# Performance work log

Hardware: AMD Instinct MI355X
Metric: run time of the kernel (lower is better)

## Reference

```python
import jax, jax.numpy as jnp
import numpy as np

B, S, D = 4, 2048, 768
H = 12
DH = D // H  # 64
DF = 2048
THETA = 10000.0
EPS = 1e-5


def setup_inputs() -> dict:
    key = jax.random.key(0)
    ks = jax.random.split(key, 8)
    sc = 0.02  # keep activations numerically tame
    return {
        "x": jax.random.normal(ks[0], (B, S, D), jnp.float32),
        "ln1_w": jnp.ones((D,), jnp.float32),
        "ln2_w": jnp.ones((D,), jnp.float32),
        "p_q": jax.random.normal(ks[1], (D, D), jnp.float32) * sc,
        "p_k": jax.random.normal(ks[2], (D, D), jnp.float32) * sc,
        "p_v": jax.random.normal(ks[3], (D, D), jnp.float32) * sc,
        "p_o": jax.random.normal(ks[4], (D, D), jnp.float32) * sc,
        "w1": jax.random.normal(ks[5], (DF, D), jnp.float32) * sc,
        "w2": jax.random.normal(ks[6], (D, DF), jnp.float32) * sc,
        "w3": jax.random.normal(ks[7], (DF, D), jnp.float32) * sc,
    }


def _rmsnorm(x, w):
    # matches torch: fp32 compute, mean-square + eps
    rms = jnp.sqrt(jnp.mean(x * x, axis=-1, keepdims=True) + EPS)
    return x / rms * w


def _rope(t):
    # t: [B, H, S, DH]; rotation per RoPE matrix: pairs (2k, 2k+1)
    pos = jnp.arange(S, dtype=jnp.float32)[:, None]            # [S,1]
    k = jnp.arange(DH // 2, dtype=jnp.float32)[None, :]        # [1,DH/2]
    ang = pos / (THETA ** (2.0 * k / DH))                      # [S,DH/2]
    cos, sin = jnp.cos(ang), jnp.sin(ang)
    t2 = t.reshape(*t.shape[:-1], DH // 2, 2)
    x0, x1 = t2[..., 0], t2[..., 1]
    o0 = cos * x0 - sin * x1
    o1 = sin * x0 + cos * x1
    return jnp.stack([o0, o1], axis=-1).reshape(t.shape)


def reference(x, ln1_w, ln2_w, p_q, p_k, p_v, p_o, w1, w2, w3):
    # --- attention sublayer ---
    h = _rmsnorm(x, ln1_w)                                     # [B,S,D]
    Wq = p_q.reshape(H, DH, D)
    Wk = p_k.reshape(H, DH, D)
    Wv = p_v.reshape(H, DH, D)
    q = _rope(jnp.einsum('bsd,hed->bhse', h, Wq))              # [B,H,S,DH]
    k = _rope(jnp.einsum('bsd,hed->bhse', h, Wk))
    v = jnp.einsum('bsd,hed->bhse', h, Wv)
    scores = jnp.einsum('bhqe,bhke->bhqk', q, k)               # [B,H,S,S]
    mask = jnp.tril(jnp.ones((S, S), bool))
    scores = jnp.where(mask, scores, -jnp.inf)
    attn = jax.nn.softmax(scores / jnp.sqrt(jnp.float32(DH)), axis=-1)
    ctx = jnp.einsum('bhqk,bhke->bhqe', attn, v)               # [B,H,S,DH]
    ctx = jnp.transpose(ctx, (0, 2, 1, 3)).reshape(B, S, D)    # [B,S,D]
    x = x + ctx @ p_o.T
    # --- SwiGLU FFN sublayer ---
    h2 = _rmsnorm(x, ln2_w)
    u1 = h2 @ w1.T
    u1 = u1 * jax.nn.sigmoid(u1)                               # SiLU
    u3 = h2 @ w3.T
    x = x + (u1 * u3) @ w2.T
    return x
```

## Files before the change

### kernel.cpp

```cpp
#include <hip/hip_runtime.h>
#include <stdint.h>

#define B_  4
#define S_  2048
#define D_  768
#define H_  12
#define DH_ 64
#define DF_ 2048
#define M_  (B_*S_)
#define NQKV 2304
#define N13  4096

typedef __attribute__((ext_vector_type(8))) short bf16x8;
typedef __attribute__((ext_vector_type(4))) short bf16x4;
typedef __attribute__((ext_vector_type(4))) float f32x4;
typedef unsigned short u16;

#if !defined(__HIP_DEVICE_COMPILE__)
  #define MFMA_K16(A,B,C) (C)
#elif __has_builtin(__builtin_amdgcn_mfma_f32_16x16x16_bf16)
  #define MFMA_K16(A,B,C) __builtin_amdgcn_mfma_f32_16x16x16_bf16((A),(B),(C),0,0,0)
#else
  #define MFMA_K16(A,B,C) __builtin_amdgcn_mfma_f32_16x16x16bf16_1k((A),(B),(C),0,0,0)
#endif

__device__ __forceinline__ float bf2f(u16 v) {
  union { uint32_t u; float f; } x; x.u = ((uint32_t)v) << 16; return x.f;
}
__device__ __forceinline__ u16 f2bf(float f) {
  union { float f; uint32_t u; } x; x.f = f;
  uint32_t r = x.u + 0x7FFFu + ((x.u >> 16) & 1u);
  return (u16)(r >> 16);
}
__device__ __forceinline__ void gl_lds16(const u16* g, u16* l) {
  __builtin_amdgcn_global_load_lds((const __attribute__((address_space(1))) uint32_t*)g,
                                   (__attribute__((address_space(3))) uint32_t*)l, 16, 0, 0);
}

__global__ __launch_bounds__(256) void cast_all_kernel(const float* __restrict__ pq,
                                                       const float* __restrict__ pk,
                                                       const float* __restrict__ pv,
                                                       const float* __restrict__ po,
                                                       const float* __restrict__ w2,
                                                       u16* __restrict__ wqkv,
                                                       u16* __restrict__ wob,
                                                       u16* __restrict__ w2b) {
  int bidx = blockIdx.x;
  const float* src; u16* dst; int off;
  if (bidx < 576)       { src = pq; dst = wqkv;           off = bidx; }
  else if (bidx < 1152) { src = pk; dst = wqkv + 589824;  off = bidx - 576; }
  else if (bidx < 1728) { src = pv; dst = wqkv + 1179648; off = bidx - 1152; }
  else if (bidx < 2304) { src = po; dst = wob;            off = bidx - 1728; }
  else                  { src = w2; dst = w2b;            off = bidx - 2304; }
  int i = off * 256 + threadIdx.x;
  float4 v = ((const float4*)src)[i];
  ushort4 o;
  o.x = f2bf(v.x); o.y = f2bf(v.y); o.z = f2bf(v.z); o.w = f2bf(v.w);
  ((ushort4*)dst)[i] = o;
}

__global__ __launch_bounds__(192) void cast_w13_kernel(const float* __restrict__ w1,
                                                       const float* __restrict__ w3,
                                                       u16* __restrict__ out) {
  int j = blockIdx.x, which = blockIdx.y;
  const float* src = (which ? w3 : w1) + (size_t)j * D_;
  int fr = (j >> 4) * 32 + (j & 15) + which * 16;
  u16* dst = out + (size_t)fr * D_;
  int t = threadIdx.x;
  float4 v = ((const float4*)src)[t];
  ushort4 o;
  o.x = f2bf(v.x); o.y = f2bf(v.y); o.z = f2bf(v.z); o.w = f2bf(v.w);
  ((ushort4*)dst)[t] = o;
}

__global__ __launch_bounds__(256) void rmsnorm_kernel(const float* __restrict__ x,
                                                      const float* __restrict__ w,
                                                      u16* __restrict__ out) {
  int row = blockIdx.x, tid = threadIdx.x;
  const float* xr = x + (size_t)row * D_;
  float v0 = xr[tid], v1 = xr[tid + 256], v2 = xr[tid + 512];
  float ss = v0 * v0 + v1 * v1 + v2 * v2;
  #pragma unroll
  for (int m = 32; m >= 1; m >>= 1) ss += __shfl_xor(ss, m, 64);
  __shared__ float red[4];
  if ((tid & 63) == 0) red[tid >> 6] = ss;
  __syncthreads();
  float tot = red[0] + red[1] + red[2] + red[3];
  float r = rsqrtf(tot * (1.0f / D_) + 1e-5f);
  u16* o = out + (size_t)row * D_;
  o[tid]       = f2bf(v0 * r * w[tid]);
  o[tid + 256] = f2bf(v1 * r * w[tid + 256]);
  o[tid + 512] = f2bf(v2 * r * w[tid + 512]);
}

template<int MT, int EPI>
__global__ __launch_bounds__(256) void gemm_bt_kernel(const u16* __restrict__ A,
                                                      const u16* __restrict__ W,
                                                      void* __restrict__ Cout,
                                                      const float* __restrict__ res,
                                                      u16* __restrict__ vTout,
                                                      int K, int N) {
  constexpr int ABELEMS = MT * 64 + 128 * 64;
  constexpr int SMELEMS = (EPI == 3 && 128 * 132 > ABELEMS) ? 128 * 132 : ABELEMS;
  __shared__ __align__(16) u16 smem[SMELEMS];
  u16* As = smem;
  u16* Bs = smem + MT * 64;
  constexpr int MI = MT / 32;
  int tid = threadIdx.x;
  int wave = tid >> 6, lane = tid & 63;
  int quad = lane >> 4, l16 = lane & 15;
  int wr = (wave >> 1) * (MT / 2), wc = (wave & 1) * 64;
  int m0 = blockIdx.y * MT, n0 = blockIdx.x * 128;
  f32x4 acc[MI][4] = {};
  for (int kt = 0; kt < K; kt += 64) {
    __syncthreads();
    #pragma unroll
    for (int i = 0; i < MT / 32; ++i) {
      int idx = i * 256 + tid;
      int r = idx >> 3, c = idx & 7;
      gl_lds16(&A[(size_t)(m0 + r) * K + kt + ((c ^ (r & 7)) * 8)], &As[(i * 256 + wave * 64) * 8]);
    }
    #pragma unroll
    for (int i = 0; i < 4; ++i) {
      int idx = i * 256 + tid;
      int r = idx >> 3, c = idx & 7;
      gl_lds16(&W[(size_t)(n0 + r) * K + kt + ((c ^ (r & 7)) * 8)], &Bs[(i * 256 + wave * 64) * 8]);
    }
    __syncthreads();
    #pragma unroll
    for (int ks = 0; ks < 2; ++ks) {
      bf16x8 af[MI], bf[4];
      int sw = ((ks * 4 + quad) ^ (l16 & 7)) * 8;
      #pragma unroll
      for (int t = 0; t < MI; ++t)
        af[t] = *(const bf16x8*)&As[(wr + t * 16 + l16) * 64 + sw];
      #pragma unroll
      for (int t = 0; t < 4; ++t)
        bf[t] = *(const bf16x8*)&Bs[(wc + t * 16 + l16) * 64 + sw];
      #pragma unroll
      for (int mt = 0; mt < MI; ++mt)
        #pragma unroll
        for (int nt = 0; nt < 4; ++nt)
          acc[mt][nt] = __builtin_amdgcn_mfma_f32_16x16x32_bf16(af[mt], bf[nt], acc[mt][nt], 0, 0, 0);
    }
  }

  if (EPI == 3 && n0 >= 1536) {
    __syncthreads();
    #pragma unroll
    for (int mt = 0; mt < MI; ++mt) {
      int sloc = wr + mt * 16 + quad * 4;
      #pragma unroll
      for (int nt = 0; nt < 4; ++nt) {
        int col = wc + nt * 16 + l16;
        ushort4 o;
        o.x = f2bf(acc[mt][nt][0]); o.y = f2bf(acc[mt][nt][1]);
        o.z = f2bf(acc[mt][nt][2]); o.w = f2bf(acc[mt][nt][3]);
        *(ushort4*)&smem[col * 132 + sloc] = o;
      }
    }
    __syncthreads();
    int b = m0 >> 11, sblk = m0 & 2047;
    #pragma unroll
    for (int i = 0; i < 8; ++i) {
      int idx = i * 256 + tid;
      int row = idx >> 4, c16 = idx & 15;
      uint4 d = *(const uint4*)&smem[row * 132 + c16 * 8];
      int vg = n0 - 1536 + row;
      int h = vg >> 6, dh = vg & 63;
      *(uint4*)&vTout[((size_t)(b * H_ + h) * 64 + dh) * (size_t)S_ + sblk + c16 * 8] = d;
    }
  } else if (EPI == 3) {
    bool isq = (n0 < 768);
    float osc = isq ? 0.18033688f : 1.0f;
    #pragma unroll
    for (int mt = 0; mt < MI; ++mt) {
      int r0 = m0 + wr + mt * 16 + quad * 4;
      int pos0 = r0 & 2047;
      #pragma unroll
      for (int nt = 0; nt < 4; ++nt) {
        int col = n0 + wc + nt * 16 + l16;
        int kk = (col & 63) >> 1;
        float freq = exp2f(-0.41524101186092035f * (float)kk);
        bool odd = (col & 1);
        #pragma unroll
        for (int r = 0; r < 4; ++r) {
          float own = acc[mt][nt][r];
          float pv = __shfl_xor(own, 1, 64);
          float ang = (float)(pos0 + r) * freq;
          float sv, cv;
          __sincosf(ang, &sv, &cv);
          float o = odd ? (sv * pv + cv * own) : (cv * own - sv * pv);
          ((u16*)Cout)[(size_t)(r0 + r) * N + col] = f2bf(o * osc);
        }
      }
    }
  } else {
    #pragma unroll
    for (int mt = 0; mt < MI; ++mt) {
      #pragma unroll
      for (int r = 0; r < 4; ++r) {
        int gr = m0 + wr + mt * 16 + quad * 4 + r;
        if (EPI == 2) {
          #pragma unroll
          for (int np = 0; np < 2; ++np) {
            float u1v = acc[mt][np * 2][r], u3v = acc[mt][np * 2 + 1][r];
            float sg = 1.0f / (1.0f + __builtin_amdgcn_exp2f(-u1v * 1.44269504f));
            float g = u1v * sg * u3v;
            int gc = (n0 >> 1) + (wave & 1) * 32 + np * 16 + l16;
            ((u16*)Cout)[(size_t)gr * (N >> 1) + gc] = f2bf(g);
          }
        } else {
          #pragma unroll
          for (int nt = 0; nt < 4; ++nt) {
            int gc = n0 + wc + nt * 16 + l16;
            size_t off = (size_t)gr * N + gc;
            float vv = acc[mt][nt][r];
            if (EPI == 1) ((float*)Cout)[off] = vv + res[off];
            else          ((u16*)Cout)[off] = f2bf(vv);
          }
        }
      }
    }
  }
}

#define FENCE() asm volatile("" ::: "memory")
#define BAR() do { FENCE(); __builtin_amdgcn_s_barrier(); FENCE(); } while (0)
#define LGKM0() do { asm volatile("s_waitcnt lgkmcnt(0)" ::: "memory"); \
                     __builtin_amdgcn_sched_barrier(0); } while (0)

template<int MH, int NH>
__device__ __forceinline__ void quad_mfma(f32x4 (&acc)[2][4][2][2],
                                          const bf16x8 (&ra)[4][2],
                                          const bf16x8 (&rb)[2][2]) {
  #pragma unroll
  for (int ks = 0; ks < 2; ++ks)
    #pragma unroll
    for (int mt = 0; mt < 4; ++mt)
      #pragma unroll
      for (int nt = 0; nt < 2; ++nt)
        acc[MH][mt][NH][nt] =
          __builtin_amdgcn_mfma_f32_16x16x32_bf16(ra[mt][ks], rb[nt][ks], acc[MH][mt][NH][nt], 0, 0, 0);
}

__device__ __forceinline__ void ld_af(bf16x8 (&rr)[4][2], const u16* base,
                                      int wrow, int l16, int quad) {
  #pragma unroll
  for (int mt = 0; mt < 4; ++mt)
    #pragma unroll
    for (int ks = 0; ks < 2; ++ks)
      rr[mt][ks] = *(const bf16x8*)&base[(wrow + mt * 16 + l16) * 64 +
                                         (((ks * 4 + quad) ^ (l16 & 7)) * 8)];
}
__device__ __forceinline__ void ld_bf(bf16x8 (&rr)[2][2], const u16* base,
                                      int wrow, int l16, int quad) {
  #pragma unroll
  for (int nt = 0; nt < 2; ++nt)
    #pragma unroll
    for (int ks = 0; ks < 2; ++ks)
      rr[nt][ks] = *(const bf16x8*)&base[(wrow + nt * 16 + l16) * 64 +
                                         (((ks * 4 + quad) ^ (l16 & 7)) * 8)];
}

template<int EPI, int K, int N>
__global__ __launch_bounds__(512, 2) void gemm256_kernel(const u16* __restrict__ A,
                                                         const u16* __restrict__ W,
                                                         void* __restrict__ Cout,
                                                         const float* __restrict__ res) {
  __shared__ __align__(16) u16 smem[2][2][2][128 * 64];
  int tid = threadIdx.x;
  int wave = tid >> 6, lane = tid & 63;
  int quad = lane >> 4, l16 = lane & 15;
  int wm = wave >> 2, wn = wave & 3;
  int m0 = blockIdx.y * 256, n0 = blockIdx.x * 256;
  constexpr int NI = (K >> 6) >> 1;

  f32x4 acc[2][4][2][2] = {};
  bf16x8 rA[4][2], rBlo[2][2], rBhi[2][2];

  int r0 = tid >> 3, c0 = tid & 7;
  int scb = (c0 ^ (r0 & 7)) * 16;
  uint32_t offA = (uint32_t)(m0 + r0) * (uint32_t)(K * 2) + (uint32_t)scb;
  uint32_t offB = (uint32_t)(n0 + r0) * (uint32_t)(K * 2) + (uint32_t)scb;

  #define STG(kof, ab, h, bufi) do {                                               \
    const char* _s = (ab) ? (const char*)W : (const char*)A;                       \
    uint32_t _o = ((ab) ? offB : offA) + (uint32_t)((kof) + (h) * (128 * K * 2));  \
    u16* _d = &smem[bufi][ab][h][wave * 512];                                      \
    gl_lds16((const u16*)(_s + _o), _d);                                           \
    gl_lds16((const u16*)(_s + _o + 64 * K * 2), _d + 4096);                       \
  } while (0)

  int wrA = wm * 64, wrB = wn * 32;

  STG(0, 0, 0, 0); STG(0, 1, 0, 0); STG(0, 1, 1, 0); STG(0, 0, 1, 0);
  STG(128, 0, 0, 1); STG(128, 1, 0, 1); STG(128, 1, 1, 1); STG(128, 0, 1, 1);
  offA += 256; offB += 256;
  asm volatile("s_waitcnt vmcnt(8)" ::: "memory");
  BAR();
  ld_af(rA,   &smem[0][0][0][0], wrA, l16, quad);
  ld_bf(rBlo, &smem[0][1][0][0], wrB, l16, quad);
  LGKM0();
  BAR();

  #define G256_ITER(MORE) do {                                                     \
                                                                     \
    ld_bf(rBhi, &smem[0][1][1][0], wrB, l16, quad);                                \
    if (MORE) STG(0, 0, 0, 0);                                                     \
    BAR(); LGKM0();                                                                \
    __builtin_amdgcn_s_setprio(1); quad_mfma<0, 0>(acc, rA, rBlo);                 \
    __builtin_amdgcn_s_setprio(0); BAR();                                          \
                                                   \
    if (MORE) STG(0, 1, 0, 0);                                                     \
    BAR(); LGKM0();                                                                \
    __builtin_amdgcn_s_setprio(1); quad_mfma<0, 1>(acc, rA, rBhi);                 \
    __builtin_amdgcn_s_setprio(0);                                                 \
    ld_af(rA, &smem[0][0][1][0], wrA, l16, quad);                                  \
    BAR();                                                                         \
                                                   \
    if (MORE) STG(0, 1, 1, 0);                                                     \
    BAR(); LGKM0();                                                                \
    __builtin_amdgcn_s_setprio(1); quad_mfma<1, 0>(acc, rA, rBlo);                 \
    __builtin_amdgcn_s_setprio(0);                                                 \
    if (MORE) asm volatile("s_waitcnt vmcnt(6)" ::: "memory");                     \
    else      asm volatile("s_waitcnt vmcnt(0)" ::: "memory");                     \
    BAR();                                                                         \
                                    \
    ld_bf(rBlo, &smem[1][1][0][0], wrB, l16, quad);                                \
    if (MORE) STG(0, 0, 1, 0);                                                     \
    BAR(); LGKM0();                                                                \
    __builtin_amdgcn_s_setprio(1); quad_mfma<1, 1>(acc, rA, rBhi);                 \
    __builtin_amdgcn_s_setprio(0);                                                 \
    ld_af(rA, &smem[1][0][0][0], wrA, l16, quad);                                  \
    BAR();                                                                         \
                                                                \
    ld_bf(rBhi, &smem[1][1][1][0], wrB, l16, quad);                                \
    if (MORE) STG(128, 0, 0, 1);                                                   \
    BAR(); LGKM0();                                                                \
    __builtin_amdgcn_s_setprio(1); quad_mfma<0, 0>(acc, rA, rBlo);                 \
    __builtin_amdgcn_s_setprio(0); BAR();                                          \
                                                   \
    if (MORE) STG(128, 1, 0, 1);                                                   \
    BAR(); LGKM0();                                                                \
    __builtin_amdgcn_s_setprio(1); quad_mfma<0, 1>(acc, rA, rBhi);                 \
    __builtin_amdgcn_s_setprio(0);                                                 \
    ld_af(rA, &smem[1][0][1][0], wrA, l16, quad);                                  \
    BAR();                                                                         \
                                                   \
    if (MORE) STG(128, 1, 1, 1);                                                   \
    BAR(); LGKM0();                                                                \
    __builtin_amdgcn_s_setprio(1); quad_mfma<1, 0>(acc, rA, rBlo);                 \
    __builtin_amdgcn_s_setprio(0);                                                 \
    if (MORE) asm volatile("s_waitcnt vmcnt(6)" ::: "memory");                     \
    else      asm volatile("s_waitcnt vmcnt(0)" ::: "memory");                     \
    BAR();                                                                         \
                                    \
    if (MORE) ld_bf(rBlo, &smem[0][1][0][0], wrB, l16, quad);                      \
    if (MORE) STG(128, 0, 1, 1);                                                   \
    BAR(); LGKM0();                                                                \
    __builtin_amdgcn_s_setprio(1); quad_mfma<1, 1>(acc, rA, rBhi);                 \
    __builtin_amdgcn_s_setprio(0);                                                 \
    if (MORE) ld_af(rA, &smem[0][0][0][0], wrA, l16, quad);                        \
    BAR();                                                                         \
  } while (0)

  #pragma unroll 1
  for (int i = 0; i < NI - 1; ++i) {
    G256_ITER(true);
    offA += 256; offB += 256;
  }
  G256_ITER(false);
  #undef G256_ITER
  #undef STG

  if (EPI == 2) {
    const int Nh = N >> 1;
    #pragma unroll
    for (int mh = 0; mh < 2; ++mh)
      #pragma unroll
      for (int mt = 0; mt < 4; ++mt)
        #pragma unroll
        for (int r = 0; r < 4; ++r) {
          int gr = m0 + mh * 128 + wm * 64 + mt * 16 + quad * 4 + r;
          #pragma unroll
          for (int nh = 0; nh < 2; ++nh) {
            float u1v = acc[mh][mt][nh][0][r], u3v = acc[mh][mt][nh][1][r];
            float sg = 1.0f / (1.0f + __builtin_amdgcn_exp2f(-u1v * 1.44269504f));
            float g = u1v * sg * u3v;
            int gc = (n0 >> 1) + nh * 64 + wn * 16 + l16;
            ((u16*)Cout)[(size_t)gr * Nh + gc] = f2bf(g);
          }
        }
  } else if (EPI == 1) {
    #pragma unroll
    for (int mh = 0; mh < 2; ++mh)
      #pragma unroll
      for (int mt = 0; mt < 4; ++mt)
        #pragma unroll
        for (int r = 0; r < 4; ++r) {
          int gr = m0 + mh * 128 + wm * 64 + mt * 16 + quad * 4 + r;
          #pragma unroll
          for (int nh = 0; nh < 2; ++nh)
            #pragma unroll
            for (int nt = 0; nt < 2; ++nt) {
              int gc = n0 + nh * 128 + wn * 32 + nt * 16 + l16;
              size_t off = (size_t)gr * N + gc;
              ((float*)Cout)[off] = acc[mh][mt][nh][nt][r] + res[off];
            }
        }
  } else {
    #pragma unroll
    for (int mh = 0; mh < 2; ++mh)
      #pragma unroll
      for (int mt = 0; mt < 4; ++mt)
        #pragma unroll
        for (int r = 0; r < 4; ++r) {
          int gr = m0 + mh * 128 + wm * 64 + mt * 16 + quad * 4 + r;
          #pragma unroll
          for (int nh = 0; nh < 2; ++nh)
            #pragma unroll
            for (int nt = 0; nt < 2; ++nt) {
              int gc = n0 + nh * 128 + wn * 32 + nt * 16 + l16;
              ((u16*)Cout)[(size_t)gr * N + gc] = f2bf(acc[mh][mt][nh][nt][r]);
            }
        }
  }
}

__global__ __launch_bounds__(256, 4) void attn_kernel(const u16* __restrict__ qkv,
                                                      const u16* __restrict__ vT,
                                                      u16* __restrict__ ctx) {
  __shared__ __align__(16) u16 Ks[128 * 64];
  __shared__ __align__(16) u16 Vt[64 * 128];
  int bh = blockIdx.x;
  int qt = 15 - blockIdx.y;
  int b = bh / H_, h = bh % H_;
  const u16* qbase = qkv + (size_t)b * S_ * NQKV + h * DH_;
  const u16* kbase = qbase + 768;
  const u16* vtb   = vT + (size_t)bh * 64 * S_;
  int tid = threadIdx.x, wave = tid >> 6, lane = tid & 63;
  int quad = lane >> 4, l16 = lane & 15;
  const float MFIX = 12.0f;

  bf16x8 qf[2][2];
  #pragma unroll
  for (int mt = 0; mt < 2; ++mt) {
    int qrow = qt * 128 + wave * 32 + mt * 16 + l16;
    qf[mt][0] = *(const bf16x8*)&qbase[(size_t)qrow * NQKV + quad * 8];
    qf[mt][1] = *(const bf16x8*)&qbase[(size_t)qrow * NQKV + 32 + quad * 8];
  }
  f32x4 oacc[2][4] = {};
  float lsum[2] = {0.f, 0.f};
  int nkt = qt + 1;
  for (int kt = 0; kt < nkt; ++kt) {
    __syncthreads();
    #pragma unroll
    for (int i = 0; i < 4; ++i) {
      int idx = i * 256 + tid;
      int r = idx >> 3, c = idx & 7;
      gl_lds16(&kbase[(size_t)(kt * 128 + r) * NQKV + ((c ^ (r & 7)) * 8)],
               &Ks[(i * 256 + wave * 64) * 8]);
    }
    #pragma unroll
    for (int i = 0; i < 4; ++i) {
      int idx = i * 256 + tid;
      int d = idx >> 4, c16 = idx & 15;
      gl_lds16(&vtb[(size_t)d * S_ + kt * 128 + ((c16 ^ (d & 15)) * 8)],
               &Vt[(i * 256 + wave * 64) * 8]);
    }
    __syncthreads();
    bool diag = (kt == nkt - 1);
    #pragma unroll
    for (int t = 0; t < 8; ++t) {
      if (diag && t > 2 * wave + 1) break;
      f32x4 sc0 = {}, sc1 = {};
      #pragma unroll
      for (int c = 0; c < 2; ++c) {
        bf16x8 kf = *(const bf16x8*)&Ks[(t * 16 + l16) * 64 + (((c * 4 + quad) ^ (l16 & 7)) * 8)];
        sc0 = __builtin_amdgcn_mfma_f32_16x16x32_bf16(kf, qf[0][c], sc0, 0, 0, 0);
        sc1 = __builtin_amdgcn_mfma_f32_16x16x32_bf16(kf, qf[1][c], sc1, 0, 0, 0);
      }
      bf16x4 pf[2];
      #pragma unroll
      for (int mt = 0; mt < 2; ++mt) {
        f32x4 sv = mt ? sc1 : sc0;
        float p[4];
        #pragma unroll
        for (int r = 0; r < 4; ++r) p[r] = __builtin_amdgcn_exp2f(sv[r] - MFIX);
        if (diag) {
          int ql = wave * 32 + mt * 16 + l16;
          #pragma unroll
          for (int r = 0; r < 4; ++r)
            if (t * 16 + quad * 4 + r > ql) p[r] = 0.f;
        }
        lsum[mt] += (p[0] + p[1]) + (p[2] + p[3]);
        uint32_t lo = ((__float_as_uint(p[0]) + 0x8000u) >> 16) |
                      ((__float_as_uint(p[1]) + 0x8000u) & 0xFFFF0000u);
        uint32_t hi = ((__float_as_uint(p[2]) + 0x8000u) >> 16) |
                      ((__float_as_uint(p[3]) + 0x8000u) & 0xFFFF0000u);
        uint2 pk; pk.x = lo; pk.y = hi;
        pf[mt] = *(bf16x4*)&pk;
      }
      #pragma unroll
      for (int n = 0; n < 4; ++n) {
        bf16x4 vf = *(const bf16x4*)&Vt[(n * 16 + l16) * 128 +
                                        (((t * 2 + (quad >> 1)) ^ l16) * 8) + (quad & 1) * 4];
        oacc[0][n] = MFMA_K16(vf, pf[0], oacc[0][n]);
        oacc[1][n] = MFMA_K16(vf, pf[1], oacc[1][n]);
      }
    }
  }
  #pragma unroll
  for (int mt = 0; mt < 2; ++mt) {
    float l = lsum[mt];
    l += __shfl_xor(l, 16, 64);
    l += __shfl_xor(l, 32, 64);
    float inv = 1.0f / l;
    int qrow = qt * 128 + wave * 32 + mt * 16 + l16;
    #pragma unroll
    for (int n = 0; n < 4; ++n) {
      ushort4 o;
      o.x = f2bf(oacc[mt][n][0] * inv);
      o.y = f2bf(oacc[mt][n][1] * inv);
      o.z = f2bf(oacc[mt][n][2] * inv);
      o.w = f2bf(oacc[mt][n][3] * inv);
      *(ushort4*)&ctx[(size_t)(b * S_ + qrow) * D_ + h * DH_ + n * 16 + quad * 4] = o;
    }
  }
}

#define WQKV_OFF 0u
#define W13_OFF  3538944u
#define W2_OFF   9830400u
#define WO_OFF   12976128u
#define HB_OFF   14155776u
#define QKV_OFF  26738688u
#define VT_OFF   64487424u
#define X1_OFF   77070336u
#define G_OFF    102236160u

extern "C" void kernel_launch(void* const* d_in, const int* in_sizes, int n_in,
                              void* d_out, int out_size, void* d_ws, size_t ws_size,
                              hipStream_t stream) {
  const float* x    = (const float*)d_in[0];
  const float* ln1w = (const float*)d_in[1];
  const float* ln2w = (const float*)d_in[2];
  const float* pq   = (const float*)d_in[3];
  const float* pk   = (const float*)d_in[4];
  const float* pv   = (const float*)d_in[5];
  const float* po   = (const float*)d_in[6];
  const float* w1   = (const float*)d_in[7];
  const float* w2   = (const float*)d_in[8];
  const float* w3   = (const float*)d_in[9];
  char* ws = (char*)d_ws;
  u16* wqkv = (u16*)(ws + WQKV_OFF);
  u16* w13b = (u16*)(ws + W13_OFF);
  u16* w2b  = (u16*)(ws + W2_OFF);
  u16* wob  = (u16*)(ws + WO_OFF);
  u16* hb   = (u16*)(ws + HB_OFF);
  u16* qkvb = (u16*)(ws + QKV_OFF);
  u16* vtb  = (u16*)(ws + VT_OFF);
  u16* cb   = (u16*)(ws + HB_OFF);
  float* x1 = (float*)(ws + X1_OFF);
  u16* h2b  = (u16*)(ws + VT_OFF);
  u16* gb   = (u16*)(ws + G_OFF);

  cast_all_kernel<<<3840, 256, 0, stream>>>(pq, pk, pv, po, w2, wqkv, wob, w2b);
  cast_w13_kernel<<<dim3(2048, 2), 192, 0, stream>>>(w1, w3, w13b);

  rmsnorm_kernel<<<M_, 256, 0, stream>>>(x, ln1w, hb);
  gemm_bt_kernel<128, 3><<<dim3(18, 64), 256, 0, stream>>>(hb, wqkv, qkvb, nullptr, vtb, 768, NQKV);
  attn_kernel<<<dim3(48, 16), 256, 0, stream>>>(qkvb, vtb, cb);
  gemm_bt_kernel<64, 1><<<dim3(6, 128), 256, 0, stream>>>(cb, wob, x1, x, nullptr, 768, 768);

  rmsnorm_kernel<<<M_, 256, 0, stream>>>(x1, ln2w, h2b);
  gemm256_kernel<2, 768, N13><<<dim3(N13 / 256, M_ / 256), 512, 0, stream>>>(h2b, w13b, gb, nullptr);
  gemm_bt_kernel<64, 1><<<dim3(6, 128), 256, 0, stream>>>(gb, w2b, (float*)d_out, x1, nullptr, 2048, 768);
}
```

Measured before the change: 345.2 us.

## Split attention query tile across eight waves with one 16-row slice each

The attention kernel now runs 512 threads (8 waves) per block instead of 256, with each wave owning 16 query rows instead of 32. K/V tile loads into LDS are spread over twice as many threads, and the causal diagonal masking is simplified to a single sub-tile per wave. This aims to balance work across waves on the diagonal tile and raise wave-level parallelism. The cost is that each K/V fragment read from LDS is reused by half as many MFMAs, which increases LDS traffic per FLOP.

```diff
diff --git a/kernel.cpp b/kernel.cpp
--- a/kernel.cpp
+++ b/kernel.cpp
@@ -428,7 +428,7 @@
   }
 }
 
-__global__ __launch_bounds__(256, 4) void attn_kernel(const u16* __restrict__ qkv,
+__global__ __launch_bounds__(512, 4) void attn_kernel(const u16* __restrict__ qkv,
                                                       const u16* __restrict__ vT,
                                                       u16* __restrict__ ctx) {
   __shared__ __align__(16) u16 Ks[128 * 64];
@@ -443,90 +443,75 @@
   int quad = lane >> 4, l16 = lane & 15;
   const float MFIX = 12.0f;
 
-  bf16x8 qf[2][2];
-  #pragma unroll
-  for (int mt = 0; mt < 2; ++mt) {
-    int qrow = qt * 128 + wave * 32 + mt * 16 + l16;
-    qf[mt][0] = *(const bf16x8*)&qbase[(size_t)qrow * NQKV + quad * 8];
-    qf[mt][1] = *(const bf16x8*)&qbase[(size_t)qrow * NQKV + 32 + quad * 8];
-  }
-  f32x4 oacc[2][4] = {};
-  float lsum[2] = {0.f, 0.f};
+  bf16x8 qf[2];
+  int qrow = qt * 128 + wave * 16 + l16;
+  qf[0] = *(const bf16x8*)&qbase[(size_t)qrow * NQKV + quad * 8];
+  qf[1] = *(const bf16x8*)&qbase[(size_t)qrow * NQKV + 32 + quad * 8];
+  f32x4 oacc[4] = {};
+  float lsum = 0.f;
   int nkt = qt + 1;
   for (int kt = 0; kt < nkt; ++kt) {
     __syncthreads();
     #pragma unroll
-    for (int i = 0; i < 4; ++i) {
-      int idx = i * 256 + tid;
+    for (int i = 0; i < 2; ++i) {
+      int idx = i * 512 + tid;
       int r = idx >> 3, c = idx & 7;
       gl_lds16(&kbase[(size_t)(kt * 128 + r) * NQKV + ((c ^ (r & 7)) * 8)],
-               &Ks[(i * 256 + wave * 64) * 8]);
-    }
-    #pragma unroll
-    for (int i = 0; i < 4; ++i) {
-      int idx = i * 256 + tid;
+               &Ks[(i * 512 + wave * 64) * 8]);
+    }
+    #pragma unroll
+    for (int i = 0; i < 2; ++i) {
+      int idx = i * 512 + tid;
       int d = idx >> 4, c16 = idx & 15;
       gl_lds16(&vtb[(size_t)d * S_ + kt * 128 + ((c16 ^ (d & 15)) * 8)],
-               &Vt[(i * 256 + wave * 64) * 8]);
+               &Vt[(i * 512 + wave * 64) * 8]);
     }
     __syncthreads();
     bool diag = (kt == nkt - 1);
     #pragma unroll
     for (int t = 0; t < 8; ++t) {
-      if (diag && t > 2 * wave + 1) break;
-      f32x4 sc0 = {}, sc1 = {};
+      if (diag && t > wave) break;
+      f32x4 sc = {};
       #pragma unroll
       for (int c = 0; c < 2; ++c) {
         bf16x8 kf = *(const bf16x8*)&Ks[(t * 16 + l16) * 64 + (((c * 4 + quad) ^ (l16 & 7)) * 8)];
-        sc0 = __builtin_amdgcn_mfma_f32_16x16x32_bf16(kf, qf[0][c], sc0, 0, 0, 0);
-        sc1 = __builtin_amdgcn_mfma_f32_16x16x32_bf16(kf, qf[1][c], sc1, 0, 0, 0);
+        sc = __builtin_amdgcn_mfma_f32_16x16x32_bf16(kf, qf[c], sc, 0, 0, 0);
       }
-      bf16x4 pf[2];
-      #pragma unroll
-      for (int mt = 0; mt < 2; ++mt) {
-        f32x4 sv = mt ? sc1 : sc0;
-        float p[4];
+      float p[4];
+      #pragma unroll
+      for (int r = 0; r < 4; ++r) p[r] = __builtin_amdgcn_exp2f(sc[r] - MFIX);
+      if (diag && t == wave) {
         #pragma unroll
-        for (int r = 0; r < 4; ++r) p[r] = __builtin_amdgcn_exp2f(sv[r] - MFIX);
-        if (diag) {
-          int ql = wave * 32 + mt * 16 + l16;
-          #pragma unroll
-          for (int r = 0; r < 4; ++r)
-            if (t * 16 + quad * 4 + r > ql) p[r] = 0.f;
-        }
-        lsum[mt] += (p[0] + p[1]) + (p[2] + p[3]);
-        uint32_t lo = ((__float_as_uint(p[0]) + 0x8000u) >> 16) |
-                      ((__float_as_uint(p[1]) + 0x8000u) & 0xFFFF0000u);
-        uint32_t hi = ((__float_as_uint(p[2]) + 0x8000u) >> 16) |
-                      ((__float_as_uint(p[3]) + 0x8000u) & 0xFFFF0000u);
-        uint2 pk; pk.x = lo; pk.y = hi;
-        pf[mt] = *(bf16x4*)&pk;
+        for (int r = 0; r < 4; ++r)
+          if (quad * 4 + r > l16) p[r] = 0.f;
       }
+      lsum += (p[0] + p[1]) + (p[2] + p[3]);
+      uint32_t lo = ((__float_as_uint(p[0]) + 0x8000u) >> 16) |
+                    ((__float_as_uint(p[1]) + 0x8000u) & 0xFFFF0000u);
+      uint32_t hi = ((__float_as_uint(p[2]) + 0x8000u) >> 16) |
+                    ((__float_as_uint(p[3]) + 0x8000u) & 0xFFFF0000u);
+      uint2 pk; pk.x = lo; pk.y = hi;
+      bf16x4 pf = *(bf16x4*)&pk;
       #pragma unroll
       for (int n = 0; n < 4; ++n) {
         bf16x4 vf = *(const bf16x4*)&Vt[(n * 16 + l16) * 128 +
                                         (((t * 2 + (quad >> 1)) ^ l16) * 8) + (quad & 1) * 4];
-        oacc[0][n] = MFMA_K16(vf, pf[0], oacc[0][n]);
-        oacc[1][n] = MFMA_K16(vf, pf[1], oacc[1][n]);
+        oacc[n] = MFMA_K16(vf, pf, oacc[n]);
       }
     }
   }
+  float l = lsum;
+  l += __shfl_xor(l, 16, 64);
+  l += __shfl_xor(l, 32, 64);
+  float inv = 1.0f / l;
   #pragma unroll
-  for (int mt = 0; mt < 2; ++mt) {
-    float l = lsum[mt];
-    l += __shfl_xor(l, 16, 64);
-    l += __shfl_xor(l, 32, 64);
-    float inv = 1.0f / l;
-    int qrow = qt * 128 + wave * 32 + mt * 16 + l16;
-    #pragma unroll
-    for (int n = 0; n < 4; ++n) {
-      ushort4 o;
-      o.x = f2bf(oacc[mt][n][0] * inv);
-      o.y = f2bf(oacc[mt][n][1] * inv);
-      o.z = f2bf(oacc[mt][n][2] * inv);
-      o.w = f2bf(oacc[mt][n][3] * inv);
-      *(ushort4*)&ctx[(size_t)(b * S_ + qrow) * D_ + h * DH_ + n * 16 + quad * 4] = o;
-    }
+  for (int n = 0; n < 4; ++n) {
+    ushort4 o;
+    o.x = f2bf(oacc[n][0] * inv);
+    o.y = f2bf(oacc[n][1] * inv);
+    o.z = f2bf(oacc[n][2] * inv);
+    o.w = f2bf(oacc[n][3] * inv);
+    *(ushort4*)&ctx[(size_t)(b * S_ + qrow) * D_ + h * DH_ + n * 16 + quad * 4] = o;
   }
 }
 
@@ -571,7 +556,7 @@
 
   rmsnorm_kernel<<<M_, 256, 0, stream>>>(x, ln1w, hb);
   gemm_bt_kernel<128, 3><<<dim3(18, 64), 256, 0, stream>>>(hb, wqkv, qkvb, nullptr, vtb, 768, NQKV);
-  attn_kernel<<<dim3(48, 16), 256, 0, stream>>>(qkvb, vtb, cb);
+  attn_kernel<<<dim3(48, 16), 512, 0, stream>>>(qkvb, vtb, cb);
   gemm_bt_kernel<64, 1><<<dim3(6, 128), 256, 0, stream>>>(cb, wob, x1, x, nullptr, 768, 768);
 
   rmsnorm_kernel<<<M_, 256, 0, stream>>>(x1, ln2w, h2b);
```

Measured after the change: 331.5 us. 1.04x faster.
